# Kernel tuning notes

Measured on AMD Instinct MI355X. Metric: run time of the kernel, lower is better.

The kernel has to match this reference:

```python
import jax, jax.numpy as jnp
import numpy as np

B, S, D, H = 4, 2048, 1024, 16
DQ = D // H  # 64


def setup_inputs() -> dict:
    key = jax.random.key(0)
    ks = jax.random.split(key, 7)
    return {
        "q": jax.random.normal(ks[0], (B, S, D), dtype=jnp.float32),
        "k": jax.random.normal(ks[1], (B, S, D), dtype=jnp.float32),
        "v": jax.random.normal(ks[2], (B, S, D), dtype=jnp.float32),
        "mask": jax.random.randint(ks[3], (B, 1, S, S), 0, 2, dtype=jnp.int32),
        "weight_q": jax.random.normal(ks[4], (H, D, DQ), dtype=jnp.float32),
        "weight_k": jax.random.normal(ks[5], (H, D, DQ), dtype=jnp.float32),
        "weight_v": jax.random.normal(ks[6], (H, D, DQ), dtype=jnp.float32),
    }


def reference(q, k, v, mask, weight_q, weight_k, weight_v):
    # Per-head projections: [b,s,d] x [h,d,q] -> [b,h,s,q]
    Q = jnp.einsum('bsd,hdq->bhsq', q, weight_q)
    K = jnp.einsum('bsd,hdq->bhsq', k, weight_k)
    V = jnp.einsum('bsd,hdq->bhsq', v, weight_v)
    scale = 1.0 / jnp.sqrt(jnp.float32(DQ))
    scores = jnp.einsum('bhsq,bhtq->bhst', Q, K) * scale  # [b,h,s,s]
    scores = jnp.where(mask == 0, jnp.float32(-1e9), scores)
    scores = jax.nn.softmax(scores, axis=-1)
    # Faithful to torch.einsum('bhss,bhsq->bhsq', ...): repeated index 's'
    # takes the DIAGONAL of the attention matrix, scaling V elementwise.
    diag = jnp.diagonal(scores, axis1=2, axis2=3)  # [b,h,s]
    x = diag[..., None] * V  # [b,h,s,dq]
    return x
```

## Files before the change

### kernel.cpp

```cpp
#include <hip/hip_runtime.h>


#define BB 4
#define SS 2048
#define DD 1024
#define HH 16
#define DQQ 64

typedef unsigned short u16;
typedef unsigned int u32;
typedef __attribute__((ext_vector_type(8))) short bf16x8;
typedef __attribute__((ext_vector_type(4))) float f32x4;

static constexpr float SCALE_L2E = 0.125f * 1.44269504f;
static constexpr float NEG9 = -1e9f;

#define MFMA16(a, b, c) __builtin_amdgcn_mfma_f32_16x16x32_bf16((a), (b), (c), 0, 0, 0)

__device__ __forceinline__ u16 bfrne(float x) {
    u32 u = __float_as_uint(x);
    return (u16)((u + 0x7fffu + ((u >> 16) & 1u)) >> 16);
}
__device__ __forceinline__ u32 pk2(float a, float b) {
    return (u32)bfrne(a) | ((u32)bfrne(b) << 16);
}
__device__ __forceinline__ float lo_f(u32 p) { return __uint_as_float(p << 16); }
__device__ __forceinline__ float hi_f(u32 p) { return __uint_as_float(p & 0xFFFF0000u); }

union U4V { u32 u[4]; bf16x8 v; uint4 q4; };

__global__ __launch_bounds__(256) void mask_pack_k(const int* __restrict__ mask,
                                                   u32* __restrict__ bits) {
    const int w = blockIdx.x * 256 + threadIdx.x;
    const long long row  = (long long)(w >> 6);
    const long long base = row * SS + (long long)((w & 63) << 5);
    const int4* mp = reinterpret_cast<const int4*>(mask + base);
    u32 v = 0;
#pragma unroll
    for (int j = 0; j < 8; ++j) {
        int4 m4 = mp[j];
        v |= (m4.x != 0 ? 1u : 0u) << (4 * j + 0);
        v |= (m4.y != 0 ? 1u : 0u) << (4 * j + 1);
        v |= (m4.z != 0 ? 1u : 0u) << (4 * j + 2);
        v |= (m4.w != 0 ? 1u : 0u) << (4 * j + 3);
    }
    bits[w] = v;
}

__global__ __launch_bounds__(256) void wsplit2_k(const float* __restrict__ W,
                                                 u16* __restrict__ Ph,
                                                 u16* __restrict__ Pl,
                                                 int has_lo, float scale) {
    const int f = blockIdx.x * 4 + (threadIdx.x >> 6);
    const int lane = threadIdx.x & 63;
    const int qtile = f >> 5, kc = f & 31;
    const int h = qtile >> 2, q = ((qtile & 3) << 4) + (lane & 15);
    const int d0 = kc * 32 + (lane >> 4) * 8;
    float x[8];
#pragma unroll
    for (int j = 0; j < 8; ++j)
        x[j] = W[((long long)h * DD + d0 + j) * DQQ + q] * scale;
    U4V hh;
    hh.u[0] = pk2(x[0], x[1]); hh.u[1] = pk2(x[2], x[3]);
    hh.u[2] = pk2(x[4], x[5]); hh.u[3] = pk2(x[6], x[7]);
    const long long base = ((long long)f << 9) + lane * 8;
    *reinterpret_cast<uint4*>(Ph + base) = hh.q4;
    if (has_lo) {
        U4V ll;
        ll.u[0] = pk2(x[0] - lo_f(hh.u[0]), x[1] - hi_f(hh.u[0]));
        ll.u[1] = pk2(x[2] - lo_f(hh.u[1]), x[3] - hi_f(hh.u[1]));
        ll.u[2] = pk2(x[4] - lo_f(hh.u[2]), x[5] - hi_f(hh.u[2]));
        ll.u[3] = pk2(x[6] - lo_f(hh.u[3]), x[7] - hi_f(hh.u[3]));
        *reinterpret_cast<uint4*>(Pl + base) = ll.q4;
    }
}

__global__ __launch_bounds__(256) void splitx_k(const float* __restrict__ X,
                                                u16* __restrict__ Xh,
                                                u16* __restrict__ Xl,
                                                int has_lo) {
    const int g = blockIdx.x * 256 + threadIdx.x;
    const int kc = g & 31;
    const int row = g >> 5;
    const float* xp = X + ((long long)row << 10) + kc * 32;
    const int lrow = row & 15;
    const long long base = (((long long)(row >> 4) * 32 + kc) << 9);
    float4 f[8];
#pragma unroll
    for (int i = 0; i < 8; ++i) f[i] = reinterpret_cast<const float4*>(xp)[i];
#pragma unroll
    for (int lg = 0; lg < 4; ++lg) {
        const float v0 = f[2 * lg].x, v1 = f[2 * lg].y, v2 = f[2 * lg].z, v3 = f[2 * lg].w;
        const float v4 = f[2 * lg + 1].x, v5 = f[2 * lg + 1].y,
                    v6 = f[2 * lg + 1].z, v7 = f[2 * lg + 1].w;
        U4V hh;
        hh.u[0] = pk2(v0, v1); hh.u[1] = pk2(v2, v3);
        hh.u[2] = pk2(v4, v5); hh.u[3] = pk2(v6, v7);
        const long long o = base + (lrow + 16 * lg) * 8;
        *reinterpret_cast<uint4*>(Xh + o) = hh.q4;
        if (has_lo) {
            U4V ll;
            ll.u[0] = pk2(v0 - lo_f(hh.u[0]), v1 - hi_f(hh.u[0]));
            ll.u[1] = pk2(v2 - lo_f(hh.u[1]), v3 - hi_f(hh.u[1]));
            ll.u[2] = pk2(v4 - lo_f(hh.u[2]), v5 - hi_f(hh.u[2]));
            ll.u[3] = pk2(v6 - lo_f(hh.u[3]), v7 - hi_f(hh.u[3]));
            *reinterpret_cast<uint4*>(Xl + o) = ll.q4;
        }
    }
}

__global__ __launch_bounds__(256) void proj_qk2_k(
        const u16* __restrict__ Xh, const u16* __restrict__ Xl,
        const u16* __restrict__ Wph, const u16* __restrict__ Wpl,
        u16* __restrict__ Oh, u16* __restrict__ Ol) {
    const int t = threadIdx.x, lane = t & 63, wid = t >> 6;
    const int lrow = lane & 15, lgrp = lane >> 4;
    const int qt0 = blockIdx.y * 8 + (wid >> 1) * 4;
    const int st0 = blockIdx.x * 8 + (wid & 1) * 4;

    f32x4 acc[4][4];
#pragma unroll
    for (int i = 0; i < 4; ++i)
#pragma unroll
        for (int j = 0; j < 4; ++j) acc[i][j] = (f32x4){0.f, 0.f, 0.f, 0.f};

#pragma unroll 2
    for (int kc = 0; kc < 32; ++kc) {
        bf16x8 Ah[4], Al[4], Bh[4], Bl[4];
#pragma unroll
        for (int mt = 0; mt < 4; ++mt) {
            const long long ab = (((long long)(qt0 + mt) * 32 + kc) << 9) + lane * 8;
            Ah[mt] = *reinterpret_cast<const bf16x8*>(Wph + ab);
            Al[mt] = *reinterpret_cast<const bf16x8*>(Wpl + ab);
        }
#pragma unroll
        for (int nt = 0; nt < 4; ++nt) {
            const long long bb = (((long long)(st0 + nt) * 32 + kc) << 9) + lane * 8;
            Bh[nt] = *reinterpret_cast<const bf16x8*>(Xh + bb);
            Bl[nt] = *reinterpret_cast<const bf16x8*>(Xl + bb);
        }
#pragma unroll
        for (int mt = 0; mt < 4; ++mt)
#pragma unroll
            for (int nt = 0; nt < 4; ++nt) {
                acc[mt][nt] = MFMA16(Ah[mt], Bh[nt], acc[mt][nt]);
                acc[mt][nt] = MFMA16(Ah[mt], Bl[nt], acc[mt][nt]);
                acc[mt][nt] = MFMA16(Al[mt], Bh[nt], acc[mt][nt]);
            }
    }

#pragma unroll
    for (int mt = 0; mt < 4; ++mt) {
        const int qtg = qt0 + mt;
        const int hh_ = qtg >> 2;
        const int qb = ((qtg & 3) << 4) + (lgrp << 2);
#pragma unroll
        for (int nt = 0; nt < 4; ++nt) {
            const int c = (st0 + nt) * 16 + lrow;
            const int b = c >> 11, s = c & 2047;
            const int bh = (b << 4) + hh_;
            const float x0 = acc[mt][nt][0], x1 = acc[mt][nt][1],
                        x2 = acc[mt][nt][2], x3 = acc[mt][nt][3];
            const u32 h01 = pk2(x0, x1), h23 = pk2(x2, x3);
            const u32 l01 = pk2(x0 - lo_f(h01), x1 - hi_f(h01));
            const u32 l23 = pk2(x2 - lo_f(h23), x3 - hi_f(h23));
            const int st = s >> 4, kcq = qb >> 5;
            const int lanep = lrow + (((qb & 31) >> 3) << 4);
            const long long oi = ((((long long)bh * 128 + st) * 2 + kcq) << 9)
                                 + lanep * 8 + (qb & 7);
            *reinterpret_cast<uint2*>(Oh + oi) = make_uint2(h01, h23);
            *reinterpret_cast<uint2*>(Ol + oi) = make_uint2(l01, l23);
        }
    }
}

__global__ __launch_bounds__(256) void proj_v2_k(
        const u16* __restrict__ Xh, const u16* __restrict__ Wph,
        u16* __restrict__ Vb) {
    const int t = threadIdx.x, lane = t & 63, wid = t >> 6;
    const int lrow = lane & 15, lgrp = lane >> 4;
    const int qt0 = blockIdx.y * 8 + (wid >> 1) * 4;
    const int st0 = blockIdx.x * 8 + (wid & 1) * 4;

    f32x4 acc[4][4];
#pragma unroll
    for (int i = 0; i < 4; ++i)
#pragma unroll
        for (int j = 0; j < 4; ++j) acc[i][j] = (f32x4){0.f, 0.f, 0.f, 0.f};

#pragma unroll 2
    for (int kc = 0; kc < 32; ++kc) {
        bf16x8 Ah[4], Bh[4];
#pragma unroll
        for (int mt = 0; mt < 4; ++mt) {
            const long long ab = (((long long)(qt0 + mt) * 32 + kc) << 9) + lane * 8;
            Ah[mt] = *reinterpret_cast<const bf16x8*>(Wph + ab);
        }
#pragma unroll
        for (int nt = 0; nt < 4; ++nt) {
            const long long bb = (((long long)(st0 + nt) * 32 + kc) << 9) + lane * 8;
            Bh[nt] = *reinterpret_cast<const bf16x8*>(Xh + bb);
        }
#pragma unroll
        for (int mt = 0; mt < 4; ++mt)
#pragma unroll
            for (int nt = 0; nt < 4; ++nt)
                acc[mt][nt] = MFMA16(Ah[mt], Bh[nt], acc[mt][nt]);
    }

#pragma unroll
    for (int mt = 0; mt < 4; ++mt) {
        const int qtg = qt0 + mt;
        const int hh_ = qtg >> 2;
        const int qb = ((qtg & 3) << 4) + (lgrp << 2);
#pragma unroll
        for (int nt = 0; nt < 4; ++nt) {
            const int c = (st0 + nt) * 16 + lrow;
            const int b = c >> 11, s = c & 2047;
            const int bh = (b << 4) + hh_;
            const u32 h01 = pk2(acc[mt][nt][0], acc[mt][nt][1]);
            const u32 h23 = pk2(acc[mt][nt][2], acc[mt][nt][3]);
            const long long oi = ((long long)bh * SS + s) * DQQ + qb;
            *reinterpret_cast<uint2*>(Vb + oi) = make_uint2(h01, h23);
        }
    }
}

__global__ __launch_bounds__(256) void attn_k(
        const u16* __restrict__ Qh, const u16* __restrict__ Ql,
        const u16* __restrict__ Kh, const u16* __restrict__ Kl,
        const u16* __restrict__ Vb, const u32* __restrict__ bits,
        float* __restrict__ out) {
    const int qt = blockIdx.x, h = blockIdx.y, b = blockIdx.z;
    const int s0 = qt * 128;
    const long long bh = b * HH + h;
    const int t = threadIdx.x, lane = t & 63, wid = t >> 6;
    const int l15 = lane & 15;

    __shared__ u16 Kst[2][2][4096];
    __shared__ float sdiag[128];
    __shared__ float dwgt[128];

    bf16x8 qfh[2][2], qfl[2][2];
#pragma unroll
    for (int mt = 0; mt < 2; ++mt)
#pragma unroll
        for (int ks = 0; ks < 2; ++ks) {
            const int stq = qt * 8 + wid * 2 + mt;
            const long long gi = (((bh * 128 + stq) * 2 + ks) << 9) + lane * 8;
            qfh[mt][ks] = *reinterpret_cast<const bf16x8*>(&Qh[gi]);
            qfl[mt][ks] = *reinterpret_cast<const bf16x8*>(&Ql[gi]);
        }

    const u32 kbase = (u32)(bh * 131072u) + (u32)t * 8u;
    bf16x8 sh[2], sl[2];
    auto loadK = [&](int cchN) {
        const u32 o = kbase + (u32)cchN * 4096u;
        sh[0] = *reinterpret_cast<const bf16x8*>(Kh + o);
        sl[0] = *reinterpret_cast<const bf16x8*>(Kl + o);
        sh[1] = *reinterpret_cast<const bf16x8*>(Kh + o + 2048u);
        sl[1] = *reinterpret_cast<const bf16x8*>(Kl + o + 2048u);
    };
    auto stageK = [&](int buf) {
#pragma unroll
        for (int i = 0; i < 2; ++i) {
            *reinterpret_cast<bf16x8*>(&Kst[buf][0][(t + i * 256) * 8]) = sh[i];
            *reinterpret_cast<bf16x8*>(&Kst[buf][1][(t + i * 256) * 8]) = sl[i];
        }
    };

    const u32* __restrict__ brow = bits + (((long long)b * SS + s0) << 6);
    u32 moff[2][4];
#pragma unroll
    for (int mt = 0; mt < 2; ++mt)
#pragma unroll
        for (int r = 0; r < 4; ++r)
            moff[mt][r] = (u32)((wid * 32 + mt * 16 + (lane >> 4) * 4 + r) << 6);

    loadK(0);
    stageK(0);

    float mrun[2][4], srun[2][4];
#pragma unroll
    for (int mt = 0; mt < 2; ++mt)
#pragma unroll
        for (int r = 0; r < 4; ++r) { mrun[mt][r] = -INFINITY; srun[mt][r] = 0.f; }

    const int cc0 = s0 >> 6;

    for (int cch = 0; cch < 32; ++cch) {
        const int cur = cch & 1;
        const int t0 = cch * 64;
        __syncthreads();
        if (cch + 1 < 32) loadK(cch + 1);

        uint2 mw[2][4];
        const u32 c2 = (u32)(cch * 2);
#pragma unroll
        for (int mt = 0; mt < 2; ++mt)
#pragma unroll
            for (int r = 0; r < 4; ++r)
                mw[mt][r] = *reinterpret_cast<const uint2*>(brow + moff[mt][r] + c2);

        bf16x8 kfh[4][2], kfl[4][2];
#pragma unroll
        for (int nt = 0; nt < 4; ++nt)
#pragma unroll
            for (int ks = 0; ks < 2; ++ks) {
                kfh[nt][ks] = *reinterpret_cast<const bf16x8*>(&Kst[cur][0][(nt * 2 + ks) * 512 + lane * 8]);
                kfl[nt][ks] = *reinterpret_cast<const bf16x8*>(&Kst[cur][1][(nt * 2 + ks) * 512 + lane * 8]);
            }

        f32x4 sc[2][4];
        const f32x4 zz = (f32x4){0.f, 0.f, 0.f, 0.f};
#pragma unroll
        for (int mt = 0; mt < 2; ++mt)
#pragma unroll
            for (int nt = 0; nt < 4; ++nt) {
                f32x4 a = MFMA16(qfh[mt][0], kfh[nt][0], zz);
                a = MFMA16(qfh[mt][1], kfh[nt][1], a);
                a = MFMA16(qfh[mt][0], kfl[nt][0], a);
                a = MFMA16(qfh[mt][1], kfl[nt][1], a);
                a = MFMA16(qfl[mt][0], kfh[nt][0], a);
                a = MFMA16(qfl[mt][1], kfh[nt][1], a);
                sc[mt][nt] = a;
            }

        const bool dchunk = (cch == cc0) || (cch == cc0 + 1);
#pragma unroll
        for (int mt = 0; mt < 2; ++mt)
#pragma unroll
            for (int r = 0; r < 4; ++r) {
                const u32 w0s = mw[mt][r].x >> l15;
                const u32 w1s = mw[mt][r].y >> l15;
                float v[4];
                v[0] = (w0s & 1u)        ? sc[mt][0][r] : NEG9;
                v[1] = (w0s & 0x10000u)  ? sc[mt][1][r] : NEG9;
                v[2] = (w1s & 1u)        ? sc[mt][2][r] : NEG9;
                v[3] = (w1s & 0x10000u)  ? sc[mt][3][r] : NEG9;
                if (dchunk) {
                    int sl_ = wid * 32 + mt * 16 + (lane >> 4) * 4 + r;
                    int cd = s0 + sl_ - t0;
#pragma unroll
                    for (int nt = 0; nt < 4; ++nt)
                        if (cd >= 0 && cd < 64 && (cd >> 4) == nt && (cd & 15) == l15)
                            sdiag[sl_] = v[nt];
                }
                float vmax = fmaxf(fmaxf(v[0], v[1]), fmaxf(v[2], v[3]));
                float mo = mrun[mt][r];
                float mn = fmaxf(mo, vmax);
                float ssum = exp2f(v[0] - mn) + exp2f(v[1] - mn) +
                             exp2f(v[2] - mn) + exp2f(v[3] - mn);
                srun[mt][r] = srun[mt][r] * exp2f(mo - mn) + ssum;
                mrun[mt][r] = mn;
            }

        if (cch + 1 < 32) stageK(cur ^ 1);
    }

#pragma unroll
    for (int mt = 0; mt < 2; ++mt)
#pragma unroll
        for (int r = 0; r < 4; ++r) {
            float mo = mrun[mt][r], so = srun[mt][r];
#pragma unroll
            for (int st = 1; st < 16; st <<= 1) {
                float m2 = __shfl_xor(mo, st, 64);
                float s2 = __shfl_xor(so, st, 64);
                float mn = fmaxf(mo, m2);
                so = so * exp2f(mo - mn) + s2 * exp2f(m2 - mn);
                mo = mn;
            }
            if (l15 == 0) {
                int sl_ = wid * 32 + mt * 16 + (lane >> 4) * 4 + r;
                dwgt[sl_] = exp2f(sdiag[sl_] - mo) / so;
            }
        }
    __syncthreads();

    const int orow = t >> 1, oc = (t & 1) * 32;
    const float w = dwgt[orow];
    const u16* vp = Vb + (bh * SS + s0 + orow) * DQQ + oc;
    float* op = out + (bh * SS + s0 + orow) * DQQ + oc;
#pragma unroll
    for (int j = 0; j < 8; ++j) {
        u32 pv = *reinterpret_cast<const u32*>(&vp[j * 4 + 0]);
        u32 pv2 = *reinterpret_cast<const u32*>(&vp[j * 4 + 2]);
        float4 o;
        o.x = lo_f(pv) * w;  o.y = hi_f(pv) * w;
        o.z = lo_f(pv2) * w; o.w = hi_f(pv2) * w;
        reinterpret_cast<float4*>(op)[j] = o;
    }
}

extern "C" void kernel_launch(void* const* d_in, const int* in_sizes, int n_in,
                              void* d_out, int out_size, void* d_ws, size_t ws_size,
                              hipStream_t stream) {
    (void)in_sizes; (void)n_in; (void)out_size; (void)ws_size;
    const float* q    = (const float*)d_in[0];
    const float* k    = (const float*)d_in[1];
    const float* v    = (const float*)d_in[2];
    const int*   mask = (const int*)d_in[3];
    const float* wq   = (const float*)d_in[4];
    const float* wk   = (const float*)d_in[5];
    const float* wv   = (const float*)d_in[6];

    const size_t NP2 = (size_t)BB * HH * SS * DQQ * 2;
    char* wsp = (char*)d_ws;
    u16* Qh = (u16*)wsp;            wsp += NP2;
    u16* Ql = (u16*)wsp;            wsp += NP2;
    u16* Kh = (u16*)wsp;            wsp += NP2;
    u16* Kl = (u16*)wsp;            wsp += NP2;
    u16* Vb = (u16*)wsp;            wsp += NP2;
    u16* Wph = (u16*)wsp;           wsp += (size_t)3 * 2048 * 512 * 2;
    u16* Wpl = (u16*)wsp;           wsp += (size_t)2 * 2048 * 512 * 2;
    u32* bits = (u32*)wsp;          wsp += (size_t)BB * SS * 64 * 4;
    u16* extra = (u16*)wsp;

    u16* Xh_q = Kh;    u16* Xl_q = Kl;
    u16* Xh_k = Vb;    u16* Xl_k = extra;
    u16* Xh_v = extra;

    mask_pack_k<<<dim3(2048), dim3(256), 0, stream>>>(mask, bits);
    wsplit2_k<<<dim3(512), dim3(256), 0, stream>>>(wq, Wph, Wpl, 1, SCALE_L2E);
    wsplit2_k<<<dim3(512), dim3(256), 0, stream>>>(wk, Wph + (1 << 20), Wpl + (1 << 20), 1, 1.0f);
    wsplit2_k<<<dim3(512), dim3(256), 0, stream>>>(wv, Wph + (2u << 20), Wph, 0, 1.0f);

    splitx_k<<<dim3(1024), dim3(256), 0, stream>>>(q, Xh_q, Xl_q, 1);
    proj_qk2_k<<<dim3(64, 8), dim3(256), 0, stream>>>(Xh_q, Xl_q, Wph, Wpl, Qh, Ql);

    splitx_k<<<dim3(1024), dim3(256), 0, stream>>>(k, Xh_k, Xl_k, 1);
    proj_qk2_k<<<dim3(64, 8), dim3(256), 0, stream>>>(Xh_k, Xl_k,
                                                      Wph + (1 << 20), Wpl + (1 << 20),
                                                      Kh, Kl);

    splitx_k<<<dim3(1024), dim3(256), 0, stream>>>(v, Xh_v, Xh_v, 0);
    proj_v2_k<<<dim3(64, 8), dim3(256), 0, stream>>>(Xh_v, Wph + (2u << 20), Vb);

    attn_k<<<dim3(16, 16, 4), dim3(256), 0, stream>>>(Qh, Ql, Kh, Kl, Vb, bits,
                                                      (float*)d_out);
}
```

Measured before the change: 388.8 us.

## Precompute diagonal score and normalize softmax against it, dropping running max

A prologue pass loads the two K chunks that hold each row's diagonal, computes the diagonal scores with MFMA and applies the mask bit, then stores them in shared memory. The main loop then sums exp2(score - diag) directly, so the output weight is 1/sum. This removes the running-max bookkeeping, the rescale exponential, and the max-merging shuffles in the final reduction. It also switches to the hardware exp2 builtin. The cost is an extra K load and MFMA prologue, and it relies on exp2 overflowing to inf to give a zero weight when another score dominates the diagonal.

After: 335.7 us. 13.7% less time.

```diff
diff --git a/kernel.cpp b/kernel.cpp
--- a/kernel.cpp
+++ b/kernel.cpp
@@ -16,6 +16,14 @@
 static constexpr float NEG9 = -1e9f;
 
 #define MFMA16(a, b, c) __builtin_amdgcn_mfma_f32_16x16x32_bf16((a), (b), (c), 0, 0, 0)
+
+__device__ __forceinline__ float ex2(float x) {
+#if __has_builtin(__builtin_amdgcn_exp2f)
+    return __builtin_amdgcn_exp2f(x);
+#else
+    return __expf(x * 0.69314718055994531f);
+#endif
+}
 
 __device__ __forceinline__ u16 bfrne(float x) {
     u32 u = __float_as_uint(x);
@@ -235,7 +243,7 @@
     const int s0 = qt * 128;
     const long long bh = b * HH + h;
     const int t = threadIdx.x, lane = t & 63, wid = t >> 6;
-    const int l15 = lane & 15;
+    const int l15 = lane & 15, lgrp = lane >> 4;
 
     __shared__ u16 Kst[2][2][4096];
     __shared__ float sdiag[128];
@@ -275,22 +283,60 @@
     for (int mt = 0; mt < 2; ++mt)
 #pragma unroll
         for (int r = 0; r < 4; ++r)
-            moff[mt][r] = (u32)((wid * 32 + mt * 16 + (lane >> 4) * 4 + r) << 6);
-
-    loadK(0);
-    stageK(0);
-
-    float mrun[2][4], srun[2][4];
+            moff[mt][r] = (u32)((wid * 32 + mt * 16 + lgrp * 4 + r) << 6);
+
+    const f32x4 zz = (f32x4){0.f, 0.f, 0.f, 0.f};
+
+    loadK(2 * qt);     stageK(0);
+    loadK(2 * qt + 1); stageK(1);
+    __syncthreads();
+    {
+        const int bufA = wid >> 1;
+        const int nt0 = (wid & 1) * 2;
+        const int cA = 2 * qt + bufA;
+#pragma unroll
+        for (int mt = 0; mt < 2; ++mt) {
+            const int ntd = nt0 + mt;
+            bf16x8 kh0 = *reinterpret_cast<const bf16x8*>(&Kst[bufA][0][(ntd * 2 + 0) * 512 + lane * 8]);
+            bf16x8 kh1 = *reinterpret_cast<const bf16x8*>(&Kst[bufA][0][(ntd * 2 + 1) * 512 + lane * 8]);
+            bf16x8 kl0 = *reinterpret_cast<const bf16x8*>(&Kst[bufA][1][(ntd * 2 + 0) * 512 + lane * 8]);
+            bf16x8 kl1 = *reinterpret_cast<const bf16x8*>(&Kst[bufA][1][(ntd * 2 + 1) * 512 + lane * 8]);
+            f32x4 a = MFMA16(qfh[mt][0], kh0, zz);
+            a = MFMA16(qfh[mt][1], kh1, a);
+            a = MFMA16(qfh[mt][0], kl0, a);
+            a = MFMA16(qfh[mt][1], kl1, a);
+            a = MFMA16(qfl[mt][0], kh0, a);
+            a = MFMA16(qfl[mt][1], kh1, a);
+#pragma unroll
+            for (int r = 0; r < 4; ++r) {
+                if (l15 == lgrp * 4 + r) {
+                    const u32 word = brow[moff[mt][r] + (u32)(cA * 2) + (u32)(ntd >> 1)];
+                    const u32 bit = (word >> ((ntd & 1) * 16 + l15)) & 1u;
+                    sdiag[wid * 32 + mt * 16 + lgrp * 4 + r] = bit ? a[r] : NEG9;
+                }
+            }
+        }
+    }
+    __syncthreads();
+
+    float sdA[2][4], nsd[2][4];
+#pragma unroll
+    for (int mt = 0; mt < 2; ++mt) {
+        float4 v4 = *reinterpret_cast<const float4*>(&sdiag[wid * 32 + mt * 16 + lgrp * 4]);
+        sdA[mt][0] = v4.x; sdA[mt][1] = v4.y; sdA[mt][2] = v4.z; sdA[mt][3] = v4.w;
+#pragma unroll
+        for (int r = 0; r < 4; ++r) nsd[mt][r] = NEG9 - sdA[mt][r];
+    }
+
+    loadK(0); stageK(0);
+    float srun[2][4];
 #pragma unroll
     for (int mt = 0; mt < 2; ++mt)
 #pragma unroll
-        for (int r = 0; r < 4; ++r) { mrun[mt][r] = -INFINITY; srun[mt][r] = 0.f; }
-
-    const int cc0 = s0 >> 6;
+        for (int r = 0; r < 4; ++r) srun[mt][r] = 0.f;
 
     for (int cch = 0; cch < 32; ++cch) {
         const int cur = cch & 1;
-        const int t0 = cch * 64;
         __syncthreads();
         if (cch + 1 < 32) loadK(cch + 1);
 
@@ -312,7 +358,6 @@
             }
 
         f32x4 sc[2][4];
-        const f32x4 zz = (f32x4){0.f, 0.f, 0.f, 0.f};
 #pragma unroll
         for (int mt = 0; mt < 2; ++mt)
 #pragma unroll
@@ -326,33 +371,22 @@
                 sc[mt][nt] = a;
             }
 
-        const bool dchunk = (cch == cc0) || (cch == cc0 + 1);
 #pragma unroll
         for (int mt = 0; mt < 2; ++mt)
 #pragma unroll
             for (int r = 0; r < 4; ++r) {
                 const u32 w0s = mw[mt][r].x >> l15;
                 const u32 w1s = mw[mt][r].y >> l15;
-                float v[4];
-                v[0] = (w0s & 1u)        ? sc[mt][0][r] : NEG9;
-                v[1] = (w0s & 0x10000u)  ? sc[mt][1][r] : NEG9;
-                v[2] = (w1s & 1u)        ? sc[mt][2][r] : NEG9;
-                v[3] = (w1s & 0x10000u)  ? sc[mt][3][r] : NEG9;
-                if (dchunk) {
-                    int sl_ = wid * 32 + mt * 16 + (lane >> 4) * 4 + r;
-                    int cd = s0 + sl_ - t0;
-#pragma unroll
-                    for (int nt = 0; nt < 4; ++nt)
-                        if (cd >= 0 && cd < 64 && (cd >> 4) == nt && (cd & 15) == l15)
-                            sdiag[sl_] = v[nt];
-                }
-                float vmax = fmaxf(fmaxf(v[0], v[1]), fmaxf(v[2], v[3]));
-                float mo = mrun[mt][r];
-                float mn = fmaxf(mo, vmax);
-                float ssum = exp2f(v[0] - mn) + exp2f(v[1] - mn) +
-                             exp2f(v[2] - mn) + exp2f(v[3] - mn);
-                srun[mt][r] = srun[mt][r] * exp2f(mo - mn) + ssum;
-                mrun[mt][r] = mn;
+                const float sd = sdA[mt][r], nd = nsd[mt][r];
+                float d0 = sc[mt][0][r] - sd;
+                float d1 = sc[mt][1][r] - sd;
+                float d2 = sc[mt][2][r] - sd;
+                float d3 = sc[mt][3][r] - sd;
+                d0 = (w0s & 1u)       ? d0 : nd;
+                d1 = (w0s & 0x10000u) ? d1 : nd;
+                d2 = (w1s & 1u)       ? d2 : nd;
+                d3 = (w1s & 0x10000u) ? d3 : nd;
+                srun[mt][r] += (ex2(d0) + ex2(d1)) + (ex2(d2) + ex2(d3));
             }
 
         if (cch + 1 < 32) stageK(cur ^ 1);
@@ -362,19 +396,12 @@
     for (int mt = 0; mt < 2; ++mt)
 #pragma unroll
         for (int r = 0; r < 4; ++r) {
-            float mo = mrun[mt][r], so = srun[mt][r];
-#pragma unroll
-            for (int st = 1; st < 16; st <<= 1) {
-                float m2 = __shfl_xor(mo, st, 64);
-                float s2 = __shfl_xor(so, st, 64);
-                float mn = fmaxf(mo, m2);
-                so = so * exp2f(mo - mn) + s2 * exp2f(m2 - mn);
-                mo = mn;
-            }
-            if (l15 == 0) {
-                int sl_ = wid * 32 + mt * 16 + (lane >> 4) * 4 + r;
-                dwgt[sl_] = exp2f(sdiag[sl_] - mo) / so;
-            }
+            float so = srun[mt][r];
+#pragma unroll
+            for (int st = 1; st < 16; st <<= 1)
+                so += __shfl_xor(so, st, 64);
+            if (l15 == 0)
+                dwgt[wid * 32 + mt * 16 + lgrp * 4 + r] = 1.0f / so;
         }
     __syncthreads();
 
```
